# Kernel tuning notes

Hardware: AMD Instinct MI355X
Metric: run time of the kernel (lower is better)

## Reference

```python
import jax, jax.numpy as jnp
import numpy as np

B, T, D, H = 64, 512, 512, 1024


def setup_inputs() -> dict:
    key = jax.random.key(0)
    k1, k2, k3, k4 = jax.random.split(key, 4)
    s_in = 1.0 / np.sqrt(D)
    s_hh = 1.0 / np.sqrt(H)
    return {
        "x": jax.random.normal(k1, (B, T, D), dtype=jnp.float32),
        "W_in": jax.random.normal(k2, (H, D), dtype=jnp.float32) * s_in,
        "b_in": jax.random.normal(k3, (H,), dtype=jnp.float32) * s_in,
        "W_hh": jax.random.normal(k4, (H, H), dtype=jnp.float32) * s_hh,
        "bias": jnp.zeros((H,), dtype=jnp.float32),
    }


def reference(x, W_in, b_in, W_hh, bias):
    # Precompute input projection for all timesteps in one big GEMM:
    # [B,T,D] @ [D,H] -> [B,T,H], plus both biases (Linear bias + extra bias param).
    xin = jnp.einsum("btd,hd->bth", x, W_in) + b_in + bias  # [B,T,H]
    xin_t = jnp.swapaxes(xin, 0, 1)  # time-major [T,B,H]

    h0 = jnp.zeros((x.shape[0], W_hh.shape[0]), dtype=x.dtype)

    def step(h, xt):
        h_new = jnp.tanh(xt + h @ W_hh.T)
        return h_new, h_new

    _, h_seq = jax.lax.scan(step, h0, xin_t)  # [T,B,H]
    return jnp.swapaxes(h_seq, 0, 1)  # [B,T,H]
```

## Files before the change

### kernel.cpp

```cpp
#include <hip/hip_runtime.h>
#include <cstdint>
#include <cstddef>

typedef unsigned short u16;
typedef unsigned int u32;
typedef unsigned long long u64;
typedef __attribute__((ext_vector_type(8))) short short8;
typedef __attribute__((ext_vector_type(4))) float f32x4;

#define MFMA16(a, b, c) __builtin_amdgcn_mfma_f32_16x16x32_bf16((a), (b), (c), 0, 0, 0)
#define SCOPE_AGENT __HIP_MEMORY_SCOPE_AGENT


static __device__ __forceinline__ u16 f2bf_rne(float f) {
  uint32_t u = __float_as_uint(f);
  u += 0x7FFFu + ((u >> 16) & 1u);
  return (u16)(u >> 16);
}
static __device__ __forceinline__ float bf2f(u16 h) {
  return __uint_as_float((uint32_t)h << 16);
}

static __device__ __forceinline__ u32 stale4(int4 d) {
  u32 s = 0;
#pragma unroll
  for (int j = 0; j < 4; ++j) {
    u32 x = ((u32*)&d)[j];
    s |= (u32)((x >> 16) == 0xFFFFu) | (u32)((x & 0xFFFFu) == 0xFFFFu);
  }
  return s;
}

static __device__ __forceinline__ int4 ld16(const u16* p, bool esc) {
  int4 r;
  if (!esc) {
    asm volatile("global_load_dwordx4 %0, %1, off sc0" : "=v"(r) : "v"(p));
  } else {
    u64 a = __hip_atomic_load((const u64*)p, __ATOMIC_RELAXED, SCOPE_AGENT);
    u64 b = __hip_atomic_load(((const u64*)p) + 1, __ATOMIC_RELAXED, SCOPE_AGENT);
    r.x = (int)(u32)a; r.y = (int)(u32)(a >> 32);
    r.z = (int)(u32)b; r.w = (int)(u32)(b >> 32);
  }
  return r;
}
static __device__ __forceinline__ u32 ldF(const u32* p, bool esc) {
  u32 r;
  if (!esc)
    asm volatile("global_load_dword %0, %1, off sc0" : "=v"(r) : "v"(p));
  else
    r = __hip_atomic_load(p, __ATOMIC_RELAXED, SCOPE_AGENT);
  return r;
}
static __device__ __forceinline__ void stH(u16* p, u32 v) {
  __hip_atomic_store(p, (u16)v, __ATOMIC_RELAXED, SCOPE_AGENT);
}
static __device__ __forceinline__ void stF(u32* p, u32 v) {
  __hip_atomic_store(p, v, __ATOMIC_RELAXED, SCOPE_AGENT);
}

static __device__ __forceinline__ void waitv0() {
  asm volatile("s_waitcnt vmcnt(0)" ::: "memory");
  __builtin_amdgcn_sched_barrier(0);
}

__global__ void split_arr(const float* __restrict__ src, u16* __restrict__ hi,
                          u16* __restrict__ lo, int n) {
  int i = blockIdx.x * blockDim.x + threadIdx.x;
  if (i >= n) return;
  float f = src[i];
  u16 h = f2bf_rne(f);
  hi[i] = h;
  lo[i] = f2bf_rne(f - bf2f(h));
}

__global__ void bias_init(const float* __restrict__ a, const float* __restrict__ b,
                          float* __restrict__ o, u32* __restrict__ cnt,
                          u32* __restrict__ flg) {
  int i = blockIdx.x * blockDim.x + threadIdx.x;
  if (i < 1024) o[i] = a[i] + b[i];
  if (i < 8)
    __hip_atomic_store(cnt + i * 64, 0u, __ATOMIC_RELAXED, SCOPE_AGENT);
  if (i < 256)
    __hip_atomic_store(flg + i, 0u, __ATOMIC_RELAXED, SCOPE_AGENT);
}

__global__ __launch_bounds__(256) void xin_gemm(
    const float* __restrict__ x, const u16* __restrict__ Bh, const u16* __restrict__ Bl,
    const float* __restrict__ bsum, float* __restrict__ out) {
  __shared__ u16 Ahi[64 * 40], Alo[64 * 40], Bhi[64 * 40], Blo[64 * 40];
  const int mb = blockIdx.y * 64, nb = blockIdx.x * 64;
  const int tid = threadIdx.x, wave = tid >> 6, lane = tid & 63;
  const int mn = lane & 15, q = lane >> 4;
  const int srow = tid >> 2, scg = tid & 3;

  f32x4 acc[4] = {};
  for (int kb = 0; kb < 512; kb += 32) {
    const float* ap = x + (size_t)(mb + srow) * 512 + kb + scg * 8;
    float4 a0 = *(const float4*)ap;
    float4 a1 = *(const float4*)(ap + 4);
    float av[8] = {a0.x, a0.y, a0.z, a0.w, a1.x, a1.y, a1.z, a1.w};
    short8 vh, vl;
#pragma unroll
    for (int j = 0; j < 8; ++j) {
      u16 h = f2bf_rne(av[j]);
      vh[j] = (short)h;
      vl[j] = (short)f2bf_rne(av[j] - bf2f(h));
    }
    short8 wh = *(const short8*)(Bh + (size_t)(nb + srow) * 512 + kb + scg * 8);
    short8 wl = *(const short8*)(Bl + (size_t)(nb + srow) * 512 + kb + scg * 8);

    __syncthreads();
    *(short8*)&Ahi[srow * 40 + scg * 8] = vh;
    *(short8*)&Alo[srow * 40 + scg * 8] = vl;
    *(short8*)&Bhi[srow * 40 + scg * 8] = wh;
    *(short8*)&Blo[srow * 40 + scg * 8] = wl;
    __syncthreads();

    short8 ah = *(const short8*)&Ahi[(wave * 16 + mn) * 40 + q * 8];
    short8 al = *(const short8*)&Alo[(wave * 16 + mn) * 40 + q * 8];
#pragma unroll
    for (int nt = 0; nt < 4; ++nt) {
      short8 bh8 = *(const short8*)&Bhi[(nt * 16 + mn) * 40 + q * 8];
      short8 bl8 = *(const short8*)&Blo[(nt * 16 + mn) * 40 + q * 8];
      acc[nt] = MFMA16(ah, bh8, acc[nt]);
      acc[nt] = MFMA16(al, bh8, acc[nt]);
      acc[nt] = MFMA16(ah, bl8, acc[nt]);
    }
  }
#pragma unroll
  for (int nt = 0; nt < 4; ++nt)
#pragma unroll
    for (int r = 0; r < 4; ++r) {
      int row = mb + wave * 16 + q * 4 + r;
      int col = nb + nt * 16 + mn;
      out[(size_t)row * 1024 + col] = acc[nt][r] + bsum[col];
    }
}

static __device__ __forceinline__ void run_steps(
    u16* hhi, u16* hlo, float* __restrict__ io, const u16* Whi, const u16* Wlo,
    float* red, const u32* myflags, u32* myflag, int b0, int c0, int wave, int mn,
    int q, int om, int on, int tid, int lane, bool esc) {
  const int kbase = wave * 256;
  u16* aplane = (mn < 8) ? hhi : hlo;
  const size_t abase = (size_t)(b0 + (mn & 7)) * 1024 + kbase + q * 8;
  const size_t iobase = (size_t)(b0 + om) * 512 * 1024 + (c0 + on);
  const size_t hword = (size_t)(b0 + om) * 1024 + (c0 + on);
  const u32* fp = myflags + (lane & 31);

  short8 bhf[8][2], blf[8][2];
#pragma unroll
  for (int kt = 0; kt < 8; ++kt) {
    const int k = kbase + kt * 32 + q * 8;
#pragma unroll
    for (int nt = 0; nt < 2; ++nt) {
      bhf[kt][nt] = *(const short8*)&Whi[(nt * 16 + mn) * 1032 + k];
      blf[kt][nt] = *(const short8*)&Wlo[(nt * 16 + mn) * 1032 + k];
    }
  }

  float xv = io[iobase];
  {
    float xn = io[iobase + 1024];
    float o = tanhf(xv);
    u16 hh = f2bf_rne(o);
    stH(hhi + (1u << 16) + hword, hh);
    stH(hlo + (1u << 16) + hword, f2bf_rne(o - bf2f(hh)));
    __syncthreads();
    if (tid == 0) stF(myflag, 1u);
    io[iobase] = o;
    xv = xn;
  }

  for (int t = 1; t < 512; ++t) {
    {
      int rounds = 0;
      for (;;) {
        u32 f = ldF(fp, esc);
        waitv0();
        if (__ballot(f >= (u32)t) == ~0ull) break;
        if (!esc && ++rounds >= 256) esc = true;
      }
    }

    const u16* pA = aplane + ((size_t)(t & 7) << 16) + abase;
    int4 v[8];
#pragma unroll
    for (int kt = 0; kt < 8; ++kt) v[kt] = ld16(pA + kt * 32, esc);
    waitv0();
    u32 sm = 0;
#pragma unroll
    for (int kt = 0; kt < 8; ++kt) sm |= stale4(v[kt]) << kt;
    int spins = 0;
    while (sm) {
      if (!esc && ++spins >= 256) esc = true;
#pragma unroll
      for (int kt = 0; kt < 8; ++kt)
        if (sm & (1u << kt)) v[kt] = ld16(pA + kt * 32, esc);
      waitv0();
      sm = 0;
#pragma unroll
      for (int kt = 0; kt < 8; ++kt) sm |= stale4(v[kt]) << kt;
    }

    float xn = 0.f;
    if (t < 511) xn = io[iobase + (size_t)(t + 1) * 1024];
    if (t < 508) {
      const size_t roff = ((size_t)((t + 4) & 7) << 16) + hword;
      stH(hhi + roff, 0xFFFFu);
      stH(hlo + roff, 0xFFFFu);
    }

    f32x4 acc[2] = {};
#pragma unroll
    for (int kt = 0; kt < 8; ++kt) {
      short8 a = *(short8*)&v[kt];
#pragma unroll
      for (int nt = 0; nt < 2; ++nt) {
        acc[nt] = MFMA16(a, bhf[kt][nt], acc[nt]);
        acc[nt] = MFMA16(a, blf[kt][nt], acc[nt]);
      }
    }

    float* rp = red + (t & 1) * 2112;
#pragma unroll
    for (int nt = 0; nt < 2; ++nt)
#pragma unroll
      for (int r = 0; r < 4; ++r)
        rp[wave * 528 + (q * 4 + r) * 33 + nt * 16 + mn] = acc[nt][r];
    __syncthreads();

    float s = 0.f;
#pragma unroll
    for (int w = 0; w < 4; ++w)
      s += rp[w * 528 + om * 33 + on] + rp[w * 528 + (om + 8) * 33 + on];
    float o = tanhf(s + xv);

    if (t < 511) {
      u16 hh = f2bf_rne(o);
      const size_t doff = ((size_t)((t + 1) & 7) << 16) + hword;
      stH(hhi + doff, hh);
      stH(hlo + doff, f2bf_rne(o - bf2f(hh)));
      __syncthreads();
      if (tid == 0) stF(myflag, (u32)(t + 1));
    }
    io[iobase + (size_t)t * 1024] = o;
    xv = xn;
  }
}

__global__ __launch_bounds__(256, 1) void rnn_steps(
    const u16* __restrict__ Wh, const u16* __restrict__ Wl, u16* hhi, u16* hlo,
    u32* cnt, u32* xccbuf, u32* flg, float* __restrict__ io) {
  extern __shared__ __align__(16) char smem[];
  u16* Whi = (u16*)smem;
  u16* Wlo = (u16*)(smem + 66048);
  float* red = (float*)(smem + 132096);

  const int tid = threadIdx.x, wave = tid >> 6, lane = tid & 63;
  const int mn = lane & 15, q = lane >> 4;
  const int wgid = blockIdx.x;
  const int bg = wgid & 7, cg = wgid >> 3;
  const int c0 = cg * 32, b0 = bg * 8;
  u32* mycnt = cnt + bg * 64;

  for (int it = tid; it < 32 * 128; it += 256) {
    int r = it >> 7, c = it & 127;
    *(short8*)&Whi[r * 1032 + c * 8] = *(const short8*)(Wh + (size_t)(c0 + r) * 1024 + c * 8);
    *(short8*)&Wlo[r * 1032 + c * 8] = *(const short8*)(Wl + (size_t)(c0 + r) * 1024 + c * 8);
  }

  const int om = tid >> 5, on = tid & 31;
  const size_t hword = (size_t)(b0 + om) * 1024 + (c0 + on);

#pragma unroll
  for (int bb = 0; bb < 8; ++bb) {
    stH(hhi + ((size_t)bb << 16) + hword, 0xFFFFu);
    stH(hlo + ((size_t)bb << 16) + hword, 0xFFFFu);
  }

  u32 xcc;
  asm volatile("s_getreg_b32 %0, hwreg(20, 0, 4)" : "=s"(xcc));
  if (tid == 0)
    __hip_atomic_store(xccbuf + wgid, xcc, __ATOMIC_RELAXED, SCOPE_AGENT);
  asm volatile("s_waitcnt vmcnt(0)" ::: "memory");
  __syncthreads();
  if (tid == 0) {
    __hip_atomic_fetch_add(mycnt, 1u, __ATOMIC_RELAXED, SCOPE_AGENT);
    while (__hip_atomic_load(mycnt, __ATOMIC_RELAXED, SCOPE_AGENT) < 32u)
      __builtin_amdgcn_s_sleep(1);
  }
  __syncthreads();

  u32 pv = __hip_atomic_load(xccbuf + bg + 8 * (lane & 31), __ATOMIC_RELAXED, SCOPE_AGENT);
  const bool fast = (__ballot(pv == xcc) == ~0ull);

  run_steps(hhi, hlo, io, Whi, Wlo, red, flg + bg * 32, flg + bg * 32 + cg, b0, c0,
            wave, mn, q, om, on, tid, lane, !fast);
}

extern "C" void kernel_launch(void* const* d_in, const int* in_sizes, int n_in, void* d_out,
                              int out_size, void* d_ws, size_t ws_size, hipStream_t stream) {
  (void)in_sizes; (void)n_in; (void)out_size; (void)ws_size;
  const float* x    = (const float*)d_in[0];
  const float* W_in = (const float*)d_in[1];
  const float* b_in = (const float*)d_in[2];
  const float* W_hh = (const float*)d_in[3];
  const float* bias = (const float*)d_in[4];
  float* out = (float*)d_out;
  char* ws = (char*)d_ws;

  u16* win_hi = (u16*)(ws);
  u16* win_lo = (u16*)(ws + (1u << 20));
  u16* whh_hi = (u16*)(ws + (2u << 20));
  u16* whh_lo = (u16*)(ws + (4u << 20));
  float* bsum = (float*)(ws + (6u << 20));
  u16* hhi    = (u16*)(ws);
  u16* hlo    = (u16*)(ws + (1u << 20));
  u32* cnt    = (u32*)(ws + (6u << 20) + 65536);
  u32* xcc    = (u32*)(ws + (6u << 20) + 65536 + 4096);
  u32* flg    = (u32*)(ws + (6u << 20) + 65536 + 8192);

  split_arr<<<dim3(524288 / 256), dim3(256), 0, stream>>>(W_in, win_hi, win_lo, 524288);
  split_arr<<<dim3(1048576 / 256), dim3(256), 0, stream>>>(W_hh, whh_hi, whh_lo, 1048576);
  bias_init<<<dim3(8), dim3(256), 0, stream>>>(b_in, bias, bsum, cnt, flg);

  xin_gemm<<<dim3(16, 512), dim3(256), 0, stream>>>(x, win_hi, win_lo, bsum, out);

  static const unsigned kSmem = 148992;
  (void)hipFuncSetAttribute((const void*)rnn_steps, hipFuncAttributeMaxDynamicSharedMemorySize,
                            (int)kSmem);
  void* args[8];
  args[0] = (void*)&whh_hi;
  args[1] = (void*)&whh_lo;
  args[2] = (void*)&hhi;
  args[3] = (void*)&hlo;
  args[4] = (void*)&cnt;
  args[5] = (void*)&xcc;
  args[6] = (void*)&flg;
  args[7] = (void*)&out;
  (void)hipLaunchCooperativeKernel((const void*)rnn_steps, dim3(256), dim3(256, 1, 1), args,
                                   kSmem, stream);
}
```

Baseline: 1.977 ms.

## Use per-wave progress flags instead of block-wide barrier before flag publish

Each wave now publishes its own progress flag after storing its slice of h, which removes the __syncthreads that preceded the single per-workgroup flag store. Consumer waves poll only the 32 flags matching their own K-slice, and the flag array grows to four entries per workgroup. The reduction barrier becomes a raw s_barrier after an LDS waitcnt. The aim is to cut intra-block serialization on the recurrent critical path, at the cost of more flag traffic and a subtler memory-ordering argument.

```diff
diff --git a/kernel.cpp b/kernel.cpp
--- a/kernel.cpp
+++ b/kernel.cpp
@@ -51,15 +51,20 @@
     r = __hip_atomic_load(p, __ATOMIC_RELAXED, SCOPE_AGENT);
   return r;
 }
-static __device__ __forceinline__ void stH(u16* p, u32 v) {
-  __hip_atomic_store(p, (u16)v, __ATOMIC_RELAXED, SCOPE_AGENT);
-}
-static __device__ __forceinline__ void stF(u32* p, u32 v) {
+static __device__ __forceinline__ void stH(u16* p, u16 v) {
+  __hip_atomic_store(p, v, __ATOMIC_RELAXED, SCOPE_AGENT);
+}
+static __device__ __forceinline__ void stFlag(u32* p, u32 v) {
   __hip_atomic_store(p, v, __ATOMIC_RELAXED, SCOPE_AGENT);
 }
 
 static __device__ __forceinline__ void waitv0() {
   asm volatile("s_waitcnt vmcnt(0)" ::: "memory");
+  __builtin_amdgcn_sched_barrier(0);
+}
+static __device__ __forceinline__ void bar_lgkm() {
+  asm volatile("s_waitcnt lgkmcnt(0)" ::: "memory");
+  __builtin_amdgcn_s_barrier();
   __builtin_amdgcn_sched_barrier(0);
 }
 
@@ -78,10 +83,8 @@
                           u32* __restrict__ flg) {
   int i = blockIdx.x * blockDim.x + threadIdx.x;
   if (i < 1024) o[i] = a[i] + b[i];
-  if (i < 8)
-    __hip_atomic_store(cnt + i * 64, 0u, __ATOMIC_RELAXED, SCOPE_AGENT);
-  if (i < 256)
-    __hip_atomic_store(flg + i, 0u, __ATOMIC_RELAXED, SCOPE_AGENT);
+  if (i < 1024) __hip_atomic_store(flg + i, 0u, __ATOMIC_RELAXED, SCOPE_AGENT);
+  if (i < 8) __hip_atomic_store(cnt + i * 64, 0u, __ATOMIC_RELAXED, SCOPE_AGENT);
 }
 
 __global__ __launch_bounds__(256) void xin_gemm(
@@ -139,14 +142,15 @@
 
 static __device__ __forceinline__ void run_steps(
     u16* hhi, u16* hlo, float* __restrict__ io, const u16* Whi, const u16* Wlo,
-    float* red, const u32* myflags, u32* myflag, int b0, int c0, int wave, int mn,
-    int q, int om, int on, int tid, int lane, bool esc) {
+    float* red, u32* bgflg, int b0, int c0, int cg, int wave, int mn,
+    int q, int om, int on, int lane, bool esc) {
   const int kbase = wave * 256;
   u16* aplane = (mn < 8) ? hhi : hlo;
   const size_t abase = (size_t)(b0 + (mn & 7)) * 1024 + kbase + q * 8;
   const size_t iobase = (size_t)(b0 + om) * 512 * 1024 + (c0 + on);
   const size_t hword = (size_t)(b0 + om) * 1024 + (c0 + on);
-  const u32* fp = myflags + (lane & 31);
+  const u32* fp = bgflg + wave * 32 + (lane & 31);
+  u32* myflag = bgflg + cg * 4 + wave;
 
   short8 bhf[8][2], blf[8][2];
 #pragma unroll
@@ -161,25 +165,25 @@
 
   float xv = io[iobase];
   {
-    float xn = io[iobase + 1024];
     float o = tanhf(xv);
     u16 hh = f2bf_rne(o);
     stH(hhi + (1u << 16) + hword, hh);
     stH(hlo + (1u << 16) + hword, f2bf_rne(o - bf2f(hh)));
-    __syncthreads();
-    if (tid == 0) stF(myflag, 1u);
+    if (lane == 0) stFlag(myflag, 1u);
     io[iobase] = o;
-    xv = xn;
+    xv = io[iobase + 1024];
   }
 
   for (int t = 1; t < 512; ++t) {
+    const u32 ut = (u32)t;
     {
       int rounds = 0;
       for (;;) {
-        u32 f = ldF(fp, esc);
+        u32 f = ut;
+        if (lane < 32) f = ldF(fp, esc);
         waitv0();
-        if (__ballot(f >= (u32)t) == ~0ull) break;
-        if (!esc && ++rounds >= 256) esc = true;
+        if (__ballot(f >= ut) == ~0ull) break;
+        if (!esc && ++rounds >= 1024) esc = true;
       }
     }
 
@@ -191,20 +195,23 @@
     u32 sm = 0;
 #pragma unroll
     for (int kt = 0; kt < 8; ++kt) sm |= stale4(v[kt]) << kt;
-    int spins = 0;
-    while (sm) {
-      if (!esc && ++spins >= 256) esc = true;
-#pragma unroll
-      for (int kt = 0; kt < 8; ++kt)
-        if (sm & (1u << kt)) v[kt] = ld16(pA + kt * 32, esc);
-      waitv0();
-      sm = 0;
-#pragma unroll
-      for (int kt = 0; kt < 8; ++kt) sm |= stale4(v[kt]) << kt;
+    {
+      int spins = 0;
+      while (__builtin_expect(sm != 0, 0)) {
+        if (!esc && ++spins >= 256) esc = true;
+#pragma unroll
+        for (int kt = 0; kt < 8; ++kt)
+          if (sm & (1u << kt)) v[kt] = ld16(pA + kt * 32, esc);
+        waitv0();
+        sm = 0;
+#pragma unroll
+        for (int kt = 0; kt < 8; ++kt) sm |= stale4(v[kt]) << kt;
+      }
     }
 
     float xn = 0.f;
     if (t < 511) xn = io[iobase + (size_t)(t + 1) * 1024];
+
     if (t < 508) {
       const size_t roff = ((size_t)((t + 4) & 7) << 16) + hword;
       stH(hhi + roff, 0xFFFFu);
@@ -228,7 +235,7 @@
 #pragma unroll
       for (int r = 0; r < 4; ++r)
         rp[wave * 528 + (q * 4 + r) * 33 + nt * 16 + mn] = acc[nt][r];
-    __syncthreads();
+    bar_lgkm();
 
     float s = 0.f;
 #pragma unroll
@@ -241,8 +248,7 @@
       const size_t doff = ((size_t)((t + 1) & 7) << 16) + hword;
       stH(hhi + doff, hh);
       stH(hlo + doff, f2bf_rne(o - bf2f(hh)));
-      __syncthreads();
-      if (tid == 0) stF(myflag, (u32)(t + 1));
+      if (lane == 0) stFlag(myflag, ut + 1);
     }
     io[iobase + (size_t)t * 1024] = o;
     xv = xn;
@@ -295,8 +301,8 @@
   u32 pv = __hip_atomic_load(xccbuf + bg + 8 * (lane & 31), __ATOMIC_RELAXED, SCOPE_AGENT);
   const bool fast = (__ballot(pv == xcc) == ~0ull);
 
-  run_steps(hhi, hlo, io, Whi, Wlo, red, flg + bg * 32, flg + bg * 32 + cg, b0, c0,
-            wave, mn, q, om, on, tid, lane, !fast);
+  run_steps(hhi, hlo, io, Whi, Wlo, red, flg + bg * 128, b0, c0, cg, wave, mn, q, om, on,
+            lane, !fast);
 }
 
 extern "C" void kernel_launch(void* const* d_in, const int* in_sizes, int n_in, void* d_out,
```

Result: slower. 3.130 ms (+58.3%).
